# Kernel optimization log

Measured on AMD Instinct MI355X. Metric: run time of the kernel, lower is better.

Reference implementation:

```python
import jax, jax.numpy as jnp
import numpy as np

K = 3  # kernel_size
K2 = K * K


def _unfold_nhwc(x):
    """x: [B,H,W,C] -> patches [B,H,W,K2,C], k index = i*K+j (matches F.unfold ordering
    after the module's reshape to (B,C,k2,H,W))."""
    B, H, W, C = x.shape
    xp = jnp.pad(x, ((0, 0), (1, 1), (1, 1), (0, 0)))  # padding=1
    patches = jnp.stack(
        [xp[:, i:i + H, j:j + W, :] for i in range(K) for j in range(K)], axis=3
    )  # [B,H,W,K2,C]
    return patches


def setup_inputs() -> dict:
    key = jax.random.key(0)
    k1, k2, k3 = jax.random.split(key, 3)
    B, H, W, C = 8, 64, 64, 256
    x = jax.random.normal(k1, (B, H, W, C), dtype=jnp.float32)
    v_w = jax.random.normal(k2, (C, C), dtype=jnp.float32) * 0.02
    proj_w = jax.random.normal(k3, (C, C), dtype=jnp.float32) * 0.02
    proj_b = jnp.zeros((C,), dtype=jnp.float32)
    return {"x": x, "v_w": v_w, "proj_w": proj_w, "proj_b": proj_b}


def reference(x, v_w, proj_w, proj_b):
    # patches: [B,H,W,K2,C]
    patches = _unfold_nhwc(x)
    # v projection (Linear, no bias): [B,H,W,K2,D]
    v = jnp.einsum("bhwkc,dc->bhwkd", patches, v_w)
    # attn = softmax(eye(k2)); output is sliced to row 0 in the original,
    # so only the first row of the constant attention matrix matters.
    attn = jax.nn.softmax(jnp.eye(K2, dtype=v.dtype), axis=-1)  # [K2,K2]
    a0 = attn[0]  # [K2]
    out = jnp.einsum("bhwkd,k->bhwd", v, a0)  # == (attn @ v)[:, 0]
    # proj Linear with bias
    out = jnp.einsum("bhwd,ed->bhwe", out, proj_w) + proj_b
    return out
```

## Files before the change

kernel.cpp:

```cpp
#include <hip/hip_runtime.h>

typedef __attribute__((ext_vector_type(8))) short short8;
typedef __attribute__((ext_vector_type(4))) float f32x4;

__device__ __forceinline__ unsigned short f2bf(float f) {
    union { float f; unsigned int u; } v; v.f = f;
    unsigned int u = v.u;
    unsigned int r = u + 0x7FFFu + ((u >> 16) & 1u);
    return (unsigned short)(r >> 16);
}

__global__ __launch_bounds__(1024) void wmat_kernel(
    const float* __restrict__ v_w, const float* __restrict__ proj_w,
    unsigned short* __restrict__ Wm)
{
    __shared__ float red[4][256];
    const int e  = blockIdx.x;
    const int c  = threadIdx.x & 255;
    const int dq = threadIdx.x >> 8;

    const float* pw = proj_w + e * 256 + dq * 64;
    const float* vv = v_w + (dq * 64) * 256 + c;

    float acc = 0.f;
#pragma unroll 8
    for (int d = 0; d < 64; ++d)
        acc = fmaf(pw[d], vv[d * 256], acc);

    red[dq][c] = acc;
    __syncthreads();
    if (threadIdx.x < 256) {
        float s = red[0][c] + red[1][c] + red[2][c] + red[3][c];
        const int wn = e >> 6, ni = (e >> 4) & 3, lrow = e & 15;
        const int kk = c >> 5, lkg = (c >> 3) & 3, c8 = c & 7;
        const int lane = lkg * 16 + lrow;
        const int idxo = ((((wn * 8 + kk) * 4 + ni) * 64 + lane) * 8) + c8;
        Wm[idxo] = f2bf(s);
    }
}

__global__ __launch_bounds__(512, 8) void fused_kernel(
    const float* __restrict__ x, const unsigned short* __restrict__ Wm,
    const float* __restrict__ proj_b, float* __restrict__ out)
{
    const int idx   = ((blockIdx.x & 7) << 7) | (blockIdx.x >> 3);
    const int b     = idx >> 7;
    const int h     = (idx >> 1) & 63;
    const int wbase = (idx & 1) * 32;
    const int t     = threadIdx.x;

    __shared__ alignas(16) char lds[32768];

    const float A1  = (float)(1.0 / 10.71828182845904523536);
    const float A0D = (float)(2.71828182845904523536 / 10.71828182845904523536) - A1;

    {
        const int strip = t >> 5;
        const int c0    = (t & 31) * 8;
        const int px0   = strip * 2;
        const int gw0   = wbase + px0;

        const f32x4 z = {0.f, 0.f, 0.f, 0.f};
        f32x4 acc[2][2];
#pragma unroll
        for (int i = 0; i < 2; ++i) { acc[i][0] = z; acc[i][1] = z; }

        for (int r = h - 1; r <= h + 1; ++r) {
            if (r < 0 || r >= 64) continue;
            const bool top = (r == h - 1);
            const float* xr = x + (((size_t)b * 64 + r) * 64) * 256 + c0;

            f32x4 pm0, pm1, pc0, pc1;
            if (gw0 == 0) { pm0 = z; pm1 = z; }
            else {
                pm0 = *(const f32x4*)(xr + (gw0 - 1) * 256);
                pm1 = *(const f32x4*)(xr + (gw0 - 1) * 256 + 4);
            }
            pc0 = *(const f32x4*)(xr + gw0 * 256);
            pc1 = *(const f32x4*)(xr + gw0 * 256 + 4);

#pragma unroll
            for (int i = 0; i < 2; ++i) {
                const int gwn = gw0 + i + 1;
                f32x4 pn0 = z, pn1 = z;
                if (gwn < 64) {
                    pn0 = *(const f32x4*)(xr + gwn * 256);
                    pn1 = *(const f32x4*)(xr + gwn * 256 + 4);
                }
                acc[i][0] += A1 * (pm0 + pc0 + pn0);
                acc[i][1] += A1 * (pm1 + pc1 + pn1);
                if (top) {
                    acc[i][0] += A0D * pm0;
                    acc[i][1] += A0D * pm1;
                }
                pm0 = pc0; pm1 = pc1; pc0 = pn0; pc1 = pn1;
            }
        }

#pragma unroll
        for (int i = 0; i < 2; ++i) {
            const int w = px0 + i;
            union { short8 v; unsigned short u[8]; } pk;
#pragma unroll
            for (int j = 0; j < 4; ++j) {
                pk.u[j]     = f2bf(acc[i][0][j]);
                pk.u[4 + j] = f2bf(acc[i][1][j]);
            }
            unsigned baddr = ((unsigned)w * 512u + (unsigned)c0 * 2u) ^ (((unsigned)(w & 7)) << 4);
            *reinterpret_cast<short8*>(lds + baddr) = pk.v;
        }
    }
    __syncthreads();

    const int w    = t >> 6;
    const int lane = t & 63;
    const int mi   = w >> 2;
    const int wn   = w & 3;
    const int lrow = lane & 15;
    const int lkg  = lane >> 4;
    const int row  = mi * 16 + lrow;

    f32x4 acc2[4];
    {
        const f32x4 z = {0.f, 0.f, 0.f, 0.f};
#pragma unroll
        for (int ni = 0; ni < 4; ++ni) acc2[ni] = z;
    }

    const unsigned abase = (unsigned)row * 512u;
    const unsigned aswz  = ((unsigned)(row & 7)) << 4;
    const unsigned short* wb = Wm + (wn << 14) + (lane << 3);

#pragma unroll
    for (int kk = 0; kk < 8; ++kk) {
        const unsigned abyte = (abase + (unsigned)(kk * 64 + lkg * 16)) ^ aswz;
        short8 a = *reinterpret_cast<const short8*>(lds + abyte);
#pragma unroll
        for (int ni = 0; ni < 4; ++ni) {
            short8 bf = *reinterpret_cast<const short8*>(wb + (kk << 11) + (ni << 9));
            acc2[ni] = __builtin_amdgcn_mfma_f32_16x16x32_bf16(bf, a, acc2[ni], 0, 0, 0);
        }
    }
    __syncthreads();

#pragma unroll
    for (int ni = 0; ni < 4; ++ni) {
        const unsigned e0 = (unsigned)(wn * 64 + ni * 16 + lkg * 4);
        unsigned baddr = ((unsigned)row * 1024u + e0 * 4u) ^ (((unsigned)(row & 7)) << 4);
        *reinterpret_cast<f32x4*>(lds + baddr) = acc2[ni];
    }
    __syncthreads();

    const f32x4 bias = *reinterpret_cast<const f32x4*>(proj_b + lane * 4);
    const size_t pxbase = (size_t)idx * 32;
#pragma unroll
    for (int j = 0; j < 4; ++j) {
        const int r = j * 8 + w;
        unsigned baddr = ((unsigned)r * 1024u + (unsigned)lane * 16u)
                         ^ (((unsigned)(r & 7)) << 4);
        f32x4 v = *reinterpret_cast<const f32x4*>(lds + baddr) + bias;
        __builtin_nontemporal_store(v, reinterpret_cast<f32x4*>(out + (pxbase + r) * 256 + lane * 4));
    }
}

extern "C" void kernel_launch(void* const* d_in, const int* in_sizes, int n_in,
                              void* d_out, int out_size, void* d_ws, size_t ws_size,
                              hipStream_t stream) {
    const float* x      = (const float*)d_in[0];
    const float* v_w    = (const float*)d_in[1];
    const float* proj_w = (const float*)d_in[2];
    const float* proj_b = (const float*)d_in[3];
    float* out = (float*)d_out;
    unsigned short* Wm = (unsigned short*)d_ws;

    wmat_kernel<<<256, 1024, 0, stream>>>(v_w, proj_w, Wm);
    fused_kernel<<<1024, 512, 0, stream>>>(x, Wm, proj_b, out);
}
```

Before: 29.41 us.

## Tile fused kernel over 8x8 pixel blocks with two M-tiles per wave

Each block now handles an 8x8 spatial tile (64 pixels) instead of a 1x32 row strip, and the grid is halved to 512 blocks. Each thread box-filters 4 consecutive pixels rather than 2, which reduces redundant halo reads of x across rows and columns. Each wave computes two 16-row MFMA tiles, so every loaded B fragment of the combined weight feeds two MFMAs. The epilogue is staged through LDS in two halves with extra barriers. The cost is more registers per thread and fewer blocks to spread over the CUs.

```diff
diff --git a/kernel.cpp b/kernel.cpp
--- a/kernel.cpp
+++ b/kernel.cpp
@@ -43,11 +43,11 @@
     const float* __restrict__ x, const unsigned short* __restrict__ Wm,
     const float* __restrict__ proj_b, float* __restrict__ out)
 {
-    const int idx   = ((blockIdx.x & 7) << 7) | (blockIdx.x >> 3);
-    const int b     = idx >> 7;
-    const int h     = (idx >> 1) & 63;
-    const int wbase = (idx & 1) * 32;
-    const int t     = threadIdx.x;
+    const int idx = ((blockIdx.x & 7) << 6) | (blockIdx.x >> 3);
+    const int b   = idx >> 6;
+    const int h0  = ((idx >> 3) & 7) * 8;
+    const int wc0 = (idx & 7) * 8;
+    const int t   = threadIdx.x;
 
     __shared__ alignas(16) char lds[32768];
 
@@ -56,19 +56,21 @@
 
     {
         const int strip = t >> 5;
+        const int rr    = strip >> 1;
+        const int q     = strip & 1;
         const int c0    = (t & 31) * 8;
-        const int px0   = strip * 2;
-        const int gw0   = wbase + px0;
+        const int gh    = h0 + rr;
+        const int gw0   = wc0 + q * 4;
 
         const f32x4 z = {0.f, 0.f, 0.f, 0.f};
-        f32x4 acc[2][2];
-#pragma unroll
-        for (int i = 0; i < 2; ++i) { acc[i][0] = z; acc[i][1] = z; }
-
-        for (int r = h - 1; r <= h + 1; ++r) {
-            if (r < 0 || r >= 64) continue;
-            const bool top = (r == h - 1);
-            const float* xr = x + (((size_t)b * 64 + r) * 64) * 256 + c0;
+        f32x4 acc[4][2];
+#pragma unroll
+        for (int i = 0; i < 4; ++i) { acc[i][0] = z; acc[i][1] = z; }
+
+        for (int gr = gh - 1; gr <= gh + 1; ++gr) {
+            if (gr < 0 || gr >= 64) continue;
+            const bool top = (gr == gh - 1);
+            const float* xr = x + (((size_t)b * 64 + gr) * 64) * 256 + c0;
 
             f32x4 pm0, pm1, pc0, pc1;
             if (gw0 == 0) { pm0 = z; pm1 = z; }
@@ -80,7 +82,7 @@
             pc1 = *(const f32x4*)(xr + gw0 * 256 + 4);
 
 #pragma unroll
-            for (int i = 0; i < 2; ++i) {
+            for (int i = 0; i < 4; ++i) {
                 const int gwn = gw0 + i + 1;
                 f32x4 pn0 = z, pn1 = z;
                 if (gwn < 64) {
@@ -98,15 +100,15 @@
         }
 
 #pragma unroll
-        for (int i = 0; i < 2; ++i) {
-            const int w = px0 + i;
+        for (int i = 0; i < 4; ++i) {
+            const int p = rr * 8 + q * 4 + i;
             union { short8 v; unsigned short u[8]; } pk;
 #pragma unroll
             for (int j = 0; j < 4; ++j) {
                 pk.u[j]     = f2bf(acc[i][0][j]);
                 pk.u[4 + j] = f2bf(acc[i][1][j]);
             }
-            unsigned baddr = ((unsigned)w * 512u + (unsigned)c0 * 2u) ^ (((unsigned)(w & 7)) << 4);
+            unsigned baddr = ((unsigned)p * 512u + (unsigned)c0 * 2u) ^ (((unsigned)(p & 7)) << 4);
             *reinterpret_cast<short8*>(lds + baddr) = pk.v;
         }
     }
@@ -114,52 +116,74 @@
 
     const int w    = t >> 6;
     const int lane = t & 63;
-    const int mi   = w >> 2;
+    const int wm   = w >> 2;
     const int wn   = w & 3;
     const int lrow = lane & 15;
     const int lkg  = lane >> 4;
-    const int row  = mi * 16 + lrow;
-
-    f32x4 acc2[4];
+
+    f32x4 acc2[2][4];
     {
         const f32x4 z = {0.f, 0.f, 0.f, 0.f};
 #pragma unroll
-        for (int ni = 0; ni < 4; ++ni) acc2[ni] = z;
-    }
-
-    const unsigned abase = (unsigned)row * 512u;
-    const unsigned aswz  = ((unsigned)(row & 7)) << 4;
+        for (int mi = 0; mi < 2; ++mi)
+#pragma unroll
+            for (int ni = 0; ni < 4; ++ni) acc2[mi][ni] = z;
+    }
+
     const unsigned short* wb = Wm + (wn << 14) + (lane << 3);
 
 #pragma unroll
     for (int kk = 0; kk < 8; ++kk) {
-        const unsigned abyte = (abase + (unsigned)(kk * 64 + lkg * 16)) ^ aswz;
-        short8 a = *reinterpret_cast<const short8*>(lds + abyte);
+        short8 a[2];
+#pragma unroll
+        for (int mi = 0; mi < 2; ++mi) {
+            const int row = wm * 32 + mi * 16 + lrow;
+            unsigned abyte = ((unsigned)row * 512u + (unsigned)(kk * 64 + lkg * 16))
+                             ^ (((unsigned)(row & 7)) << 4);
+            a[mi] = *reinterpret_cast<const short8*>(lds + abyte);
+        }
 #pragma unroll
         for (int ni = 0; ni < 4; ++ni) {
             short8 bf = *reinterpret_cast<const short8*>(wb + (kk << 11) + (ni << 9));
-            acc2[ni] = __builtin_amdgcn_mfma_f32_16x16x32_bf16(bf, a, acc2[ni], 0, 0, 0);
+#pragma unroll
+            for (int mi = 0; mi < 2; ++mi)
+                acc2[mi][ni] = __builtin_amdgcn_mfma_f32_16x16x32_bf16(bf, a[mi], acc2[mi][ni], 0, 0, 0);
         }
     }
     __syncthreads();
 
-#pragma unroll
-    for (int ni = 0; ni < 4; ++ni) {
-        const unsigned e0 = (unsigned)(wn * 64 + ni * 16 + lkg * 4);
-        unsigned baddr = ((unsigned)row * 1024u + e0 * 4u) ^ (((unsigned)(row & 7)) << 4);
-        *reinterpret_cast<f32x4*>(lds + baddr) = acc2[ni];
-    }
-    __syncthreads();
-
     const f32x4 bias = *reinterpret_cast<const f32x4*>(proj_b + lane * 4);
-    const size_t pxbase = (size_t)idx * 32;
-#pragma unroll
-    for (int j = 0; j < 4; ++j) {
-        const int r = j * 8 + w;
-        unsigned baddr = ((unsigned)r * 1024u + (unsigned)lane * 16u)
-                         ^ (((unsigned)(r & 7)) << 4);
-        f32x4 v = *reinterpret_cast<const f32x4*>(lds + baddr) + bias;
-        __builtin_nontemporal_store(v, reinterpret_cast<f32x4*>(out + (pxbase + r) * 256 + lane * 4));
+
+#pragma unroll
+    for (int half = 0; half < 2; ++half) {
+        if (wm == half) {
+#pragma unroll
+            for (int mi = 0; mi < 2; ++mi) {
+#pragma unroll
+                for (int ni = 0; ni < 4; ++ni) {
+                    const int trow = mi * 16 + lrow;
+                    const unsigned e0 = (unsigned)(wn * 64 + ni * 16 + lkg * 4);
+                    unsigned baddr = ((unsigned)trow * 1024u + e0 * 4u)
+                                     ^ (((unsigned)(trow & 7)) << 4);
+                    *reinterpret_cast<f32x4*>(lds + baddr) = acc2[mi][ni];
+                }
+            }
+        }
+        __syncthreads();
+
+#pragma unroll
+        for (int j = 0; j < 4; ++j) {
+            const int r = j * 8 + w;
+            const int p = half * 32 + r;
+            const int gh = h0 + (p >> 3);
+            const int gw = wc0 + (p & 7);
+            unsigned baddr = ((unsigned)r * 1024u + (unsigned)lane * 16u)
+                             ^ (((unsigned)(r & 7)) << 4);
+            f32x4 v = *reinterpret_cast<const f32x4*>(lds + baddr) + bias;
+            __builtin_nontemporal_store(
+                v, reinterpret_cast<f32x4*>(out + (((size_t)b * 64 + gh) * 64 + gw) * 256 + lane * 4));
+        }
+        __syncthreads();
     }
 }
 
@@ -174,5 +198,5 @@
     unsigned short* Wm = (unsigned short*)d_ws;
 
     wmat_kernel<<<256, 1024, 0, stream>>>(v_w, proj_w, Wm);
-    fused_kernel<<<1024, 512, 0, stream>>>(x, Wm, proj_b, out);
-}
+    fused_kernel<<<512, 512, 0, stream>>>(x, Wm, proj_b, out);
+}
```

After: 55.34 us. 1.88x slower.
